# Kernel tuning notes

Measured on AMD Instinct MI355X. Metric: run time of the kernel, lower is better.

Reference implementation:

```python
import jax, jax.numpy as jnp
import numpy as np

D_NODE = 128
D_EDGE = 128
D_HID = 128
D_OUT = 128
N_NODES = 50000
N_EDGES = 500000
LN_EPS = 1e-5


def setup_inputs() -> dict:
    key = jax.random.key(0)
    ks = jax.random.split(key, 10)
    d_cat = 2 * D_NODE + D_EDGE  # 384
    inv = lambda d: 1.0 / np.sqrt(d)
    return {
        "efeat": jax.random.normal(ks[0], (N_EDGES, D_EDGE), jnp.float32),
        "nfeat": jax.random.normal(ks[1], (N_NODES, D_NODE), jnp.float32),
        "src": jax.random.randint(ks[2], (N_EDGES,), 0, N_NODES),
        "dst": jax.random.randint(ks[3], (N_EDGES,), 0, N_NODES),
        # MLP params: Linear(d_cat, hid) -> SiLU -> Linear(hid, out) -> LayerNorm(out)
        "W1": jax.random.uniform(ks[4], (d_cat, D_HID), jnp.float32, -inv(d_cat), inv(d_cat)),
        "b1": jnp.zeros((D_HID,), jnp.float32),
        "W2": jax.random.uniform(ks[5], (D_HID, D_OUT), jnp.float32, -inv(D_HID), inv(D_HID)),
        "b2": jnp.zeros((D_OUT,), jnp.float32),
        "gamma": jnp.ones((D_OUT,), jnp.float32),
        "beta": jnp.zeros((D_OUT,), jnp.float32),
    }


def _layernorm(x, gamma, beta):
    mu = jnp.mean(x, axis=-1, keepdims=True)
    var = jnp.mean(jnp.square(x - mu), axis=-1, keepdims=True)
    return (x - mu) * jax.lax.rsqrt(var + LN_EPS) * gamma + beta


def reference(efeat, nfeat, src, dst, W1, b1, W2, b2, gamma, beta):
    # gather source/target node feats per edge and concat with edge feats: [E, 2*Dn+De]
    cat_feat = jnp.concatenate([efeat, nfeat[src], nfeat[dst]], axis=-1)
    h = jax.nn.silu(cat_feat @ W1 + b1)          # [E, hid]
    out = _layernorm(h @ W2 + b2, gamma, beta)    # [E, out]
    efeat_new = out + efeat                        # residual
    return (efeat_new, nfeat)
```

## Files before the change

kernel.cpp:

```cpp
#include <hip/hip_runtime.h>
#include <hip/hip_bf16.h>

#define N_EDGES 500000
#define N_NODES 50000
#define NT ((N_EDGES + 63) / 64)
#define GRID 256
#define LN_EPS 1e-5f

typedef __attribute__((ext_vector_type(8))) short bf16x8;
typedef __attribute__((ext_vector_type(4))) short bf16x4;
typedef __attribute__((ext_vector_type(4))) float f32x4;

static __device__ __forceinline__ short f2bf(float f) {
  return __builtin_bit_cast(short, __float2bfloat16(f));
}
static __device__ __forceinline__ float bf2f(short s) {
  unsigned u = ((unsigned)(unsigned short)s) << 16;
  return __builtin_bit_cast(float, u);
}
static __device__ __forceinline__ void gload16(const void* g, void* l) {
  __builtin_amdgcn_global_load_lds(
      (const __attribute__((address_space(1))) unsigned int*)g,
      (__attribute__((address_space(3))) unsigned int*)l, 16, 0, 0);
}
static __device__ __forceinline__ void bar_lds() {
  __builtin_amdgcn_sched_barrier(0);
  asm volatile("s_waitcnt lgkmcnt(0)" ::: "memory");
  __builtin_amdgcn_s_barrier();
  __builtin_amdgcn_sched_barrier(0);
}
static __device__ __forceinline__ void bar_vm4() {
  __builtin_amdgcn_sched_barrier(0);
  asm volatile("s_waitcnt vmcnt(4) lgkmcnt(0)" ::: "memory");
  __builtin_amdgcn_s_barrier();
  __builtin_amdgcn_sched_barrier(0);
}

__global__ void convert_kernel(const float* __restrict__ W1,
                               const float* __restrict__ W2,
                               const float* __restrict__ nfeat,
                               short* __restrict__ w1t, short* __restrict__ w2t,
                               short* __restrict__ nbf, float* __restrict__ outn) {
  const int step = gridDim.x * blockDim.x;
  const int t0 = blockIdx.x * blockDim.x + threadIdx.x;
  for (int i = t0; i < 384 * 128; i += step) {
    int n = i / 384, k = i - n * 384;
    w1t[i] = f2bf(W1[k * 128 + n]);
  }
  for (int i = t0; i < 128 * 128; i += step) {
    int n = i >> 7, k = i & 127;
    w2t[i] = f2bf(W2[k * 128 + n]);
  }
  for (int i = t0; i < N_NODES * 128 / 4; i += step) {
    f32x4 v = *(const f32x4*)(nfeat + (size_t)i * 4);
    short o4[4];
#pragma unroll
    for (int q = 0; q < 4; ++q) o4[q] = f2bf(v[q]);
    *(unsigned long long*)(nbf + (size_t)i * 4) = *(unsigned long long*)o4;
    *(f32x4*)(outn + (size_t)i * 4) = v;
  }
}

__global__ __launch_bounds__(512, 2) void edge_mlp_pipelined(
    const float* __restrict__ efeat, const short* __restrict__ nbf,
    const int* __restrict__ src, const int* __restrict__ dst,
    const short* __restrict__ w1t, const short* __restrict__ w2t,
    const float* __restrict__ b1, const float* __restrict__ b2,
    const float* __restrict__ gamma, const float* __restrict__ beta,
    float* __restrict__ out) {
  __shared__ __align__(16) char smem[136192];
  char* Hb = smem + 98304;
  char* xb = smem + 114688;
  float* scr = (float*)(smem + 131072);
  float* gb = (float*)(smem + 135168);

  const int tid = threadIdx.x;
  const int lane = tid & 63;
  const int w = tid >> 6;
  const int lrow = lane & 15;
  const int kgrp = (lane >> 4) & 3;
  const int col = w * 16 + lrow;
  const float b1v = b1[col], b2v = b2[col];
  if (tid < 256) gb[tid] = tid < 128 ? gamma[tid] : beta[tid - 128];

  int grow[4], goff[4], gseg[4];
#pragma unroll
  for (int i = 0; i < 4; ++i) {
    int F = w * 4096 + i * 1024 + lane * 16;
    grow[i] = F >> 9;
    int win = F & 511;
    gseg[i] = win >> 8;
    goff[i] = (win & 255) ^ ((grow[i] & 15) << 4);
  }
  const int frow = tid >> 3;
  const int fcb = tid & 7;
  const int fswz = (frow & 15) << 4;

  f32x4 S[4];
  auto stage_S = [&](int t) {
    int e = t * 64 + frow;
    e = e < N_EDGES ? e : (N_EDGES - 1);
#pragma unroll
    for (int it = 0; it < 4; ++it)
      S[it] = *(const f32x4*)(efeat + (size_t)e * 128 + (fcb + it * 8) * 4);
  };
  auto write_ef = [&](char* buf) {
#pragma unroll
    for (int it = 0; it < 4; ++it) {
      bf16x4 v;
#pragma unroll
      for (int j = 0; j < 4; ++j) v[j] = f2bf(S[it][j]);
      *(bf16x4*)(buf + frow * 256 + (((fcb + it * 8) * 8) ^ fswz)) = v;
    }
  };
  int idxN[4];
  auto load_idx = [&](int t, int* ix) {
#pragma unroll
    for (int i = 0; i < 4; ++i) {
      int e = t * 64 + grow[i];
      e = e < N_EDGES ? e : (N_EDGES - 1);
      ix[i] = gseg[i] ? dst[e] : src[e];
    }
  };
  auto issue_g = [&](char* buf, const int* ix) {
#pragma unroll
    for (int i = 0; i < 4; ++i)
      gload16((const char*)nbf + (size_t)ix[i] * 256 + goff[i],
              buf + 16384 + w * 4096 + i * 1024);
  };

  const int t0 = blockIdx.x;
  char* cur = smem;
  char* nxt = smem + 49152;
  {
    int ix0[4];
    load_idx(t0, ix0);
    stage_S(t0);
    write_ef(cur);
    issue_g(cur, ix0);
    load_idx(t0 + GRID, idxN);
  }

  for (int t = t0; t < NT; t += GRID) {
    stage_S(t + GRID);
    issue_g(nxt, idxN);
    bar_vm4();
    load_idx(t + 2 * GRID, idxN);

    bf16x8 B1[12];
#pragma unroll
    for (int ks = 0; ks < 12; ++ks)
      B1[ks] = *(const bf16x8*)(w1t + col * 384 + ks * 32 + kgrp * 8);
    f32x4 acc[4];
#pragma unroll
    for (int m = 0; m < 4; ++m) acc[m] = (f32x4)0.f;
#pragma unroll
    for (int ks = 0; ks < 12; ++ks) {
      bf16x8 a[4];
#pragma unroll
      for (int m = 0; m < 4; ++m) {
        int row = m * 16 + lrow;
        int sw = (row & 15) << 4;
        a[m] = (ks < 4)
                   ? *(const bf16x8*)(cur + row * 256 + ((ks * 64 + kgrp * 16) ^ sw))
                   : *(const bf16x8*)(cur + 16384 + row * 512 +
                                      (((ks - 4) * 64 + kgrp * 16) ^ sw));
      }
#pragma unroll
      for (int m = 0; m < 4; ++m)
        acc[m] = __builtin_amdgcn_mfma_f32_16x16x32_bf16(a[m], B1[ks], acc[m], 0, 0, 0);
    }

#pragma unroll
    for (int m = 0; m < 4; ++m)
#pragma unroll
      for (int r = 0; r < 4; ++r) {
        float x = acc[m][r] + b1v;
        float h = x / (1.f + __expf(-x));
        int row = m * 16 + kgrp * 4 + r;
        *(short*)(Hb + row * 256 + ((col * 2) ^ ((row & 15) << 4))) = f2bf(h);
      }
    bar_lds();

    bf16x8 B2[4];
#pragma unroll
    for (int ks = 0; ks < 4; ++ks)
      B2[ks] = *(const bf16x8*)(w2t + col * 128 + ks * 32 + kgrp * 8);
    f32x4 acc2[4];
#pragma unroll
    for (int m = 0; m < 4; ++m) acc2[m] = (f32x4)0.f;
#pragma unroll
    for (int ks = 0; ks < 4; ++ks) {
      bf16x8 a[4];
#pragma unroll
      for (int m = 0; m < 4; ++m) {
        int row = m * 16 + lrow;
        a[m] = *(const bf16x8*)(Hb + row * 256 +
                                ((ks * 64 + kgrp * 16) ^ ((row & 15) << 4)));
      }
#pragma unroll
      for (int m = 0; m < 4; ++m)
        acc2[m] = __builtin_amdgcn_mfma_f32_16x16x32_bf16(a[m], B2[ks], acc2[m], 0, 0, 0);
    }

#pragma unroll
    for (int m = 0; m < 4; ++m)
#pragma unroll
      for (int r = 0; r < 4; ++r) {
        float x = acc2[m][r] + b2v;
        float s1 = x, s2 = x * x;
#pragma unroll
        for (int off = 1; off < 16; off <<= 1) {
          s1 += __shfl_xor(s1, off, 64);
          s2 += __shfl_xor(s2, off, 64);
        }
        int row = m * 16 + kgrp * 4 + r;
        if (lrow == 0) {
          scr[row * 16 + w * 2] = s1;
          scr[row * 16 + w * 2 + 1] = s2;
        }
        *(short*)(xb + row * 256 + ((col * 2) ^ ((row & 15) << 4))) = f2bf(x);
      }
    bar_lds();

    {
      float s1 = 0.f, s2 = 0.f;
#pragma unroll
      for (int q = 0; q < 8; ++q) {
        s1 += scr[frow * 16 + q * 2];
        s2 += scr[frow * 16 + q * 2 + 1];
      }
      float mu = s1 * (1.f / 128.f);
      float var = s2 * (1.f / 128.f) - mu * mu;
      float rs = rsqrtf(var + LN_EPS);
      int e = t * 64 + frow;
      if (e < N_EDGES) {
        float* op = out + (size_t)e * 128;
#pragma unroll
        for (int it = 0; it < 4; ++it) {
          int c4 = fcb + it * 8;
          bf16x4 xv = *(const bf16x4*)(xb + frow * 256 + ((c4 * 8) ^ fswz));
          bf16x4 rv = *(const bf16x4*)(cur + frow * 256 + ((c4 * 8) ^ fswz));
          f32x4 g = *(const f32x4*)(gb + c4 * 4);
          f32x4 be = *(const f32x4*)(gb + 128 + c4 * 4);
          f32x4 o;
#pragma unroll
          for (int j = 0; j < 4; ++j)
            o[j] = (bf2f(xv[j]) - mu) * rs * g[j] + be[j] + bf2f(rv[j]);
          *(f32x4*)(op + c4 * 4) = o;
        }
      }
    }
    write_ef(nxt);
    char* tmp = cur; cur = nxt; nxt = tmp;
  }
  asm volatile("s_waitcnt vmcnt(0)" ::: "memory");
}

__global__ void edge_simple(const float* __restrict__ efeat, const float* __restrict__ nfeat,
                            const int* __restrict__ src, const int* __restrict__ dst,
                            const float* __restrict__ W1, const float* __restrict__ b1,
                            const float* __restrict__ W2, const float* __restrict__ b2,
                            const float* __restrict__ g, const float* __restrict__ be,
                            float* __restrict__ out) {
  int e = blockIdx.x, j = threadIdx.x;
  __shared__ float cat[384], h[128], red[128];
  cat[j] = efeat[(size_t)e * 128 + j];
  cat[128 + j] = nfeat[(size_t)src[e] * 128 + j];
  cat[256 + j] = nfeat[(size_t)dst[e] * 128 + j];
  __syncthreads();
  float s = b1[j];
  for (int k = 0; k < 384; ++k) s += cat[k] * W1[k * 128 + j];
  h[j] = s / (1.f + expf(-s));
  __syncthreads();
  float o = b2[j];
  for (int k = 0; k < 128; ++k) o += h[k] * W2[k * 128 + j];
  red[j] = o;
  __syncthreads();
  __shared__ float mu, rs;
  if (j == 0) {
    float s1 = 0, s2 = 0;
    for (int k = 0; k < 128; ++k) { s1 += red[k]; s2 += red[k] * red[k]; }
    mu = s1 / 128.f;
    rs = rsqrtf(s2 / 128.f - mu * mu + LN_EPS);
  }
  __syncthreads();
  out[(size_t)e * 128 + j] = (o - mu) * rs * g[j] + be[j] + efeat[(size_t)e * 128 + j];
}

extern "C" void kernel_launch(void* const* d_in, const int* in_sizes, int n_in,
                              void* d_out, int out_size, void* d_ws, size_t ws_size,
                              hipStream_t stream) {
  const float* efeat = (const float*)d_in[0];
  const float* nfeat = (const float*)d_in[1];
  const int* src = (const int*)d_in[2];
  const int* dst = (const int*)d_in[3];
  const float* W1 = (const float*)d_in[4];
  const float* b1 = (const float*)d_in[5];
  const float* W2 = (const float*)d_in[6];
  const float* b2 = (const float*)d_in[7];
  const float* gamma = (const float*)d_in[8];
  const float* beta = (const float*)d_in[9];
  float* out = (float*)d_out;

  short* w1t = (short*)d_ws;
  short* w2t = w1t + 384 * 128;
  short* nbf = w2t + 128 * 128;
  const size_t need =
      (size_t)(384 * 128 + 128 * 128 + (size_t)N_NODES * 128) * sizeof(short);

  if (ws_size >= need) {
    convert_kernel<<<1024, 256, 0, stream>>>(W1, W2, nfeat, w1t, w2t, nbf,
                                             out + (size_t)N_EDGES * 128);
    edge_mlp_pipelined<<<GRID, 512, 0, stream>>>(efeat, nbf, src, dst, w1t, w2t,
                                                 b1, b2, gamma, beta, out);
  } else {
    hipMemcpyAsync(out + (size_t)N_EDGES * 128, nfeat,
                   (size_t)N_NODES * 128 * sizeof(float),
                   hipMemcpyDeviceToDevice, stream);
    edge_simple<<<N_EDGES, 128, 0, stream>>>(efeat, nfeat, src, dst, W1, b1, W2,
                                             b2, gamma, beta, out);
  }
}
```

Measured before the change: 340.3 us.

## Retile waves 2x4 with register-resident weights and row-local LayerNorm stats

Each of the eight waves now owns a 32x32 output tile (2 M by 2 N fragments) instead of a 16-column strip over all 64 rows. This halves the A-fragment LDS reads per wave, and the W1/W2 fragments are loaded into registers once before the persistent loop instead of on every tile. The LayerNorm statistics are now computed in the epilogue from the bf16 x values in LDS, using an 8-lane shuffle reduction, which removes the scratch buffer and the 16-lane shuffle chains. The wait threshold is relaxed to vmcnt(8) because the load counts changed. The risk is high register pressure from 128 held weight registers at 2 blocks per CU, and the statistics now come from bf16-rounded values.

After: 333.4 us. 2.0% less time.

```diff
diff --git a/kernel.cpp b/kernel.cpp
--- a/kernel.cpp
+++ b/kernel.cpp
@@ -29,9 +29,9 @@
   __builtin_amdgcn_s_barrier();
   __builtin_amdgcn_sched_barrier(0);
 }
-static __device__ __forceinline__ void bar_vm4() {
+static __device__ __forceinline__ void bar_vm8() {
   __builtin_amdgcn_sched_barrier(0);
-  asm volatile("s_waitcnt vmcnt(4) lgkmcnt(0)" ::: "memory");
+  asm volatile("s_waitcnt vmcnt(8) lgkmcnt(0)" ::: "memory");
   __builtin_amdgcn_s_barrier();
   __builtin_amdgcn_sched_barrier(0);
 }
@@ -68,20 +68,34 @@
     const float* __restrict__ b1, const float* __restrict__ b2,
     const float* __restrict__ gamma, const float* __restrict__ beta,
     float* __restrict__ out) {
-  __shared__ __align__(16) char smem[136192];
+  __shared__ __align__(16) char smem[132096];
   char* Hb = smem + 98304;
   char* xb = smem + 114688;
-  float* scr = (float*)(smem + 131072);
-  float* gb = (float*)(smem + 135168);
+  float* gb = (float*)(smem + 131072);
 
   const int tid = threadIdx.x;
   const int lane = tid & 63;
   const int w = tid >> 6;
+  const int wm = w >> 2;
+  const int wn = w & 3;
   const int lrow = lane & 15;
   const int kgrp = (lane >> 4) & 3;
-  const int col = w * 16 + lrow;
-  const float b1v = b1[col], b2v = b2[col];
   if (tid < 256) gb[tid] = tid < 128 ? gamma[tid] : beta[tid - 128];
+
+  bf16x8 B1[12][2], B2[4][2];
+  float b1v[2], b2v[2];
+#pragma unroll
+  for (int n = 0; n < 2; ++n) {
+    const int c = wn * 32 + n * 16 + lrow;
+    b1v[n] = b1[c];
+    b2v[n] = b2[c];
+#pragma unroll
+    for (int ks = 0; ks < 12; ++ks)
+      B1[ks][n] = *(const bf16x8*)(w1t + c * 384 + ks * 32 + kgrp * 8);
+#pragma unroll
+    for (int ks = 0; ks < 4; ++ks)
+      B2[ks][n] = *(const bf16x8*)(w2t + c * 128 + ks * 32 + kgrp * 8);
+  }
 
   int grow[4], goff[4], gseg[4];
 #pragma unroll
@@ -144,22 +158,20 @@
   for (int t = t0; t < NT; t += GRID) {
     stage_S(t + GRID);
     issue_g(nxt, idxN);
-    bar_vm4();
+    bar_vm8();
     load_idx(t + 2 * GRID, idxN);
 
-    bf16x8 B1[12];
-#pragma unroll
-    for (int ks = 0; ks < 12; ++ks)
-      B1[ks] = *(const bf16x8*)(w1t + col * 384 + ks * 32 + kgrp * 8);
-    f32x4 acc[4];
-#pragma unroll
-    for (int m = 0; m < 4; ++m) acc[m] = (f32x4)0.f;
+    f32x4 acc[2][2];
+#pragma unroll
+    for (int m = 0; m < 2; ++m)
+#pragma unroll
+      for (int n = 0; n < 2; ++n) acc[m][n] = (f32x4)0.f;
 #pragma unroll
     for (int ks = 0; ks < 12; ++ks) {
-      bf16x8 a[4];
-#pragma unroll
-      for (int m = 0; m < 4; ++m) {
-        int row = m * 16 + lrow;
+      bf16x8 a[2];
+#pragma unroll
+      for (int m = 0; m < 2; ++m) {
+        int row = wm * 32 + m * 16 + lrow;
         int sw = (row & 15) << 4;
         a[m] = (ks < 4)
                    ? *(const bf16x8*)(cur + row * 256 + ((ks * 64 + kgrp * 16) ^ sw))
@@ -167,69 +179,79 @@
                                       (((ks - 4) * 64 + kgrp * 16) ^ sw));
       }
 #pragma unroll
-      for (int m = 0; m < 4; ++m)
-        acc[m] = __builtin_amdgcn_mfma_f32_16x16x32_bf16(a[m], B1[ks], acc[m], 0, 0, 0);
-    }
-
-#pragma unroll
-    for (int m = 0; m < 4; ++m)
-#pragma unroll
-      for (int r = 0; r < 4; ++r) {
-        float x = acc[m][r] + b1v;
-        float h = x / (1.f + __expf(-x));
-        int row = m * 16 + kgrp * 4 + r;
-        *(short*)(Hb + row * 256 + ((col * 2) ^ ((row & 15) << 4))) = f2bf(h);
-      }
+      for (int m = 0; m < 2; ++m)
+#pragma unroll
+        for (int n = 0; n < 2; ++n)
+          acc[m][n] = __builtin_amdgcn_mfma_f32_16x16x32_bf16(a[m], B1[ks][n],
+                                                              acc[m][n], 0, 0, 0);
+    }
+
+#pragma unroll
+    for (int m = 0; m < 2; ++m)
+#pragma unroll
+      for (int n = 0; n < 2; ++n)
+#pragma unroll
+        for (int r = 0; r < 4; ++r) {
+          float x = acc[m][n][r] + b1v[n];
+          float h = x / (1.f + __expf(-x));
+          int row = wm * 32 + m * 16 + kgrp * 4 + r;
+          int col = wn * 32 + n * 16 + lrow;
+          *(short*)(Hb + row * 256 + ((col * 2) ^ ((row & 15) << 4))) = f2bf(h);
+        }
     bar_lds();
 
-    bf16x8 B2[4];
-#pragma unroll
-    for (int ks = 0; ks < 4; ++ks)
-      B2[ks] = *(const bf16x8*)(w2t + col * 128 + ks * 32 + kgrp * 8);
-    f32x4 acc2[4];
-#pragma unroll
-    for (int m = 0; m < 4; ++m) acc2[m] = (f32x4)0.f;
+    f32x4 acc2[2][2];
+#pragma unroll
+    for (int m = 0; m < 2; ++m)
+#pragma unroll
+      for (int n = 0; n < 2; ++n) acc2[m][n] = (f32x4)0.f;
 #pragma unroll
     for (int ks = 0; ks < 4; ++ks) {
-      bf16x8 a[4];
-#pragma unroll
-      for (int m = 0; m < 4; ++m) {
-        int row = m * 16 + lrow;
+      bf16x8 a[2];
+#pragma unroll
+      for (int m = 0; m < 2; ++m) {
+        int row = wm * 32 + m * 16 + lrow;
         a[m] = *(const bf16x8*)(Hb + row * 256 +
                                 ((ks * 64 + kgrp * 16) ^ ((row & 15) << 4)));
       }
 #pragma unroll
-      for (int m = 0; m < 4; ++m)
-        acc2[m] = __builtin_amdgcn_mfma_f32_16x16x32_bf16(a[m], B2[ks], acc2[m], 0, 0, 0);
-    }
-
-#pragma unroll
-    for (int m = 0; m < 4; ++m)
-#pragma unroll
-      for (int r = 0; r < 4; ++r) {
-        float x = acc2[m][r] + b2v;
-        float s1 = x, s2 = x * x;
-#pragma unroll
-        for (int off = 1; off < 16; off <<= 1) {
-          s1 += __shfl_xor(s1, off, 64);
-          s2 += __shfl_xor(s2, off, 64);
+      for (int m = 0; m < 2; ++m)
+#pragma unroll
+        for (int n = 0; n < 2; ++n)
+          acc2[m][n] = __builtin_amdgcn_mfma_f32_16x16x32_bf16(a[m], B2[ks][n],
+                                                               acc2[m][n], 0, 0, 0);
+    }
+
+#pragma unroll
+    for (int m = 0; m < 2; ++m)
+#pragma unroll
+      for (int n = 0; n < 2; ++n)
+#pragma unroll
+        for (int r = 0; r < 4; ++r) {
+          float x = acc2[m][n][r] + b2v[n];
+          int row = wm * 32 + m * 16 + kgrp * 4 + r;
+          int col = wn * 32 + n * 16 + lrow;
+          *(short*)(xb + row * 256 + ((col * 2) ^ ((row & 15) << 4))) = f2bf(x);
         }
-        int row = m * 16 + kgrp * 4 + r;
-        if (lrow == 0) {
-          scr[row * 16 + w * 2] = s1;
-          scr[row * 16 + w * 2 + 1] = s2;
+    bar_lds();
+
+    {
+      bf16x4 xv[4];
+      float s1 = 0.f, s2 = 0.f;
+#pragma unroll
+      for (int it = 0; it < 4; ++it) {
+        int c4 = fcb + it * 8;
+        xv[it] = *(const bf16x4*)(xb + frow * 256 + ((c4 * 8) ^ fswz));
+#pragma unroll
+        for (int j = 0; j < 4; ++j) {
+          float f = bf2f(xv[it][j]);
+          s1 += f;
+          s2 += f * f;
         }
-        *(short*)(xb + row * 256 + ((col * 2) ^ ((row & 15) << 4))) = f2bf(x);
       }
-    bar_lds();
-
-    {
-      float s1 = 0.f, s2 = 0.f;
-#pragma unroll
-      for (int q = 0; q < 8; ++q) {
-        s1 += scr[frow * 16 + q * 2];
-        s2 += scr[frow * 16 + q * 2 + 1];
-      }
+      s1 += __shfl_xor(s1, 1, 64); s2 += __shfl_xor(s2, 1, 64);
+      s1 += __shfl_xor(s1, 2, 64); s2 += __shfl_xor(s2, 2, 64);
+      s1 += __shfl_xor(s1, 4, 64); s2 += __shfl_xor(s2, 4, 64);
       float mu = s1 * (1.f / 128.f);
       float var = s2 * (1.f / 128.f) - mu * mu;
       float rs = rsqrtf(var + LN_EPS);
@@ -239,14 +261,13 @@
 #pragma unroll
         for (int it = 0; it < 4; ++it) {
           int c4 = fcb + it * 8;
-          bf16x4 xv = *(const bf16x4*)(xb + frow * 256 + ((c4 * 8) ^ fswz));
           bf16x4 rv = *(const bf16x4*)(cur + frow * 256 + ((c4 * 8) ^ fswz));
           f32x4 g = *(const f32x4*)(gb + c4 * 4);
           f32x4 be = *(const f32x4*)(gb + 128 + c4 * 4);
           f32x4 o;
 #pragma unroll
           for (int j = 0; j < 4; ++j)
-            o[j] = (bf2f(xv[j]) - mu) * rs * g[j] + be[j] + bf2f(rv[j]);
+            o[j] = (bf2f(xv[it][j]) - mu) * rs * g[j] + be[j] + bf2f(rv[j]);
           *(f32x4*)(op + c4 * 4) = o;
         }
       }
```
